# Kernel optimization log

Hardware: AMD Instinct MI355X
Metric: run time of the kernel (lower is better)

Reference implementation:

```python
import jax, jax.numpy as jnp
import numpy as np

B, T, D = 4, 1024, 2048      # batch, tokens, d_model (= Linear out_features)
N, S, H = 8, 8, 8            # n_concepts, gate_rank, degen_rank
ETA = 1.0


def setup_inputs() -> dict:
    key = jax.random.key(0)
    ks = jax.random.split(key, 9)
    return {
        "x": jax.random.normal(ks[0], (B, T, D), jnp.float32),
        # selector params (kaiming-ish then / d_model^2 -> small); use /D for nontrivial values
        "select_weight": jax.random.normal(ks[1], (N, D, S), jnp.float32) / D,
        "select_mean_diff": jax.random.normal(ks[2], (N, D), jnp.float32) / D,
        "imp_center": jax.random.normal(ks[3], (N,), jnp.float32),
        "imp_slope": jax.random.normal(ks[4], (N,), jnp.float32) * 5.0,
        "lora_update": jax.random.normal(ks[5], (N, D, H), jnp.float32) * 0.02,
        "lora_degen": jax.random.normal(ks[6], (N, D, H), jnp.float32) * 0.02,
        "bias_w": jax.random.normal(ks[7], (N, D), jnp.float32) * 0.02,
        "debias_w": jax.random.normal(ks[8], (N, D), jnp.float32) * 0.02,
    }


def reference(x, select_weight, select_mean_diff, imp_center, imp_slope,
              lora_update, lora_degen, bias_w, debias_w):
    # ---- SimpleSelectorOutProp ----
    # x: [B,T,D]; x_diff: [B,N,T,D]  (x.unsqueeze(1) - mean_diff[None,:,None,:])
    x_diff = x[:, None, :, :] - select_mean_diff[None, :, None, :]
    x_diff = x_diff / jnp.linalg.norm(x_diff, axis=3, keepdims=True)
    # cont: [B,N,T,S] = einsum('nds,bntd->bnts')**2
    cont = jnp.einsum('nds,bntd->bnts', select_weight, x_diff) ** 2
    score = cont.sum(axis=-1)                                   # [B,N,T]
    gate = jax.nn.sigmoid(imp_slope[None, :, None] * (score - imp_center[None, :, None]))
    sel_scale = gate.max(axis=1)[..., None]                     # [B,T,1] (max over concepts)
    sel_idx = gate.argmax(axis=1)                               # [B,T] int (top-1 concept)

    # ---- top-1 concept gather + low-rank update ----
    debias = jnp.take(debias_w, sel_idx, axis=0)                # [B,T,D]
    bias = jnp.take(bias_w, sel_idx, axis=0)                    # [B,T,D]
    upd = jnp.take(lora_update, sel_idx, axis=0)                # [B,T,D,H]
    dgn = jnp.take(lora_degen, sel_idx, axis=0)                 # [B,T,D,H]

    x_debias = x - debias
    mod_x = jnp.einsum('btdh,btd->bth', upd, x_debias)          # [B,T,H]
    degen_up = jnp.einsum('btdh,bth->btd', dgn, mod_x)          # [B,T,D]
    mod_x_bias = ETA * (bias + degen_up)

    # gated residual blend: (1 - s) * x + s * mod_x_bias
    return (1.0 - sel_scale) * x + sel_scale * mod_x_bias
```

## Files before the change

### kernel.cpp

```cpp
#include <hip/hip_runtime.h>
#include <math.h>

typedef unsigned short u16;
typedef unsigned int   u32;
typedef unsigned long long u64;
typedef __attribute__((ext_vector_type(4))) unsigned short u16x4;
typedef __attribute__((ext_vector_type(8))) unsigned short bf16x8;
typedef __attribute__((ext_vector_type(8))) short sh8;
typedef __attribute__((ext_vector_type(4))) float f32x4;

#define BT     4096
#define D      2048
#define NC     8
#define NCOL   144
#define NW     16
#define KR     (D / NW)
#define TPB    16
#define LPAD   (NCOL + 4)

__device__ __forceinline__ float bf2f(u16 v) {
    u32 u = ((u32)v) << 16;
    float f; __builtin_memcpy(&f, &u, 4); return f;
}
__device__ __forceinline__ u16 f2bf(float f) {
    u32 u; __builtin_memcpy(&u, &f, 4);
    u += 0x7fffu + ((u >> 16) & 1);
    return (u16)(u >> 16);
}

__device__ __forceinline__ int detect_fp32(const void* xv) {
    const u16* p = (const u16*)xv;
    int l = threadIdx.x & 63;
    bool bad = false;
#pragma unroll
    for (int i = 0; i < 4; i++) {
        float v = bf2f(p[l * 4 + i]);
        if (!(fabsf(v) < 1e4f)) bad = true;
    }
    return __ballot(bad) != 0ull;
}

template<int DT> struct IO;
template<> struct IO<0> {
    static __device__ __forceinline__ float ld1(const void* p, size_t i) {
        return bf2f(((const u16*)p)[i]);
    }
    static __device__ __forceinline__ void ld4(const void* p, size_t i, float* o) {
        u16x4 v = *(const u16x4*)((const u16*)p + i);
#pragma unroll
        for (int k = 0; k < 4; k++) o[k] = bf2f(v[k]);
    }
    static __device__ __forceinline__ void ld8(const void* p, size_t i, float* o) {
        bf16x8 v = *(const bf16x8*)((const u16*)p + i);
#pragma unroll
        for (int k = 0; k < 8; k++) o[k] = bf2f(v[k]);
    }
    static __device__ __forceinline__ void st4(void* p, size_t i, const float* v) {
        u16x4 o;
#pragma unroll
        for (int k = 0; k < 4; k++) o[k] = f2bf(v[k]);
        *(u16x4*)((u16*)p + i) = o;
    }
    static __device__ __forceinline__ u16 ldbf(const void* p, size_t i) {
        return ((const u16*)p)[i];
    }
    static __device__ __forceinline__ sh8 afrag(const void* p, size_t i) {
        return *(const sh8*)((const u16*)p + i);
    }
};
template<> struct IO<1> {
    static __device__ __forceinline__ float ld1(const void* p, size_t i) {
        return ((const float*)p)[i];
    }
    static __device__ __forceinline__ void ld4(const void* p, size_t i, float* o) {
        f32x4 a = *(const f32x4*)((const float*)p + i);
#pragma unroll
        for (int k = 0; k < 4; k++) o[k] = a[k];
    }
    static __device__ __forceinline__ void ld8(const void* p, size_t i, float* o) {
        f32x4 a = *(const f32x4*)((const float*)p + i);
        f32x4 b = *(const f32x4*)((const float*)p + i + 4);
#pragma unroll
        for (int k = 0; k < 4; k++) { o[k] = a[k]; o[4 + k] = b[k]; }
    }
    static __device__ __forceinline__ void st4(void* p, size_t i, const float* v) {
        f32x4 a;
#pragma unroll
        for (int k = 0; k < 4; k++) a[k] = v[k];
        *(f32x4*)((float*)p + i) = a;
    }
    static __device__ __forceinline__ u16 ldbf(const void* p, size_t i) {
        return f2bf(((const float*)p)[i]);
    }
    static __device__ __forceinline__ sh8 afrag(const void* p, size_t i) {
        f32x4 a = *(const f32x4*)((const float*)p + i);
        f32x4 b = *(const f32x4*)((const float*)p + i + 4);
        sh8 r;
#pragma unroll
        for (int k = 0; k < 4; k++) {
            r[k]     = (short)f2bf(a[k]);
            r[4 + k] = (short)f2bf(b[k]);
        }
        return r;
    }
};

template<int DT>
__device__ __forceinline__ void prep_part(const void* selW, const void* upd,
                                          const void* mu, u16* __restrict__ WtT) {
    int idx = blockIdx.x * 256 + threadIdx.x;
    int j = idx >> 8, d0 = (idx & 255) * 8;
    bf16x8 v;
    if (j < 64) {
        int n = j >> 3, s = j & 7;
#pragma unroll
        for (int i = 0; i < 8; i++) v[i] = IO<DT>::ldbf(selW, ((size_t)n * D + d0 + i) * 8 + s);
    } else if (j < 128) {
        int n = (j - 64) >> 3, h = j & 7;
#pragma unroll
        for (int i = 0; i < 8; i++) v[i] = IO<DT>::ldbf(upd, ((size_t)n * D + d0 + i) * 8 + h);
    } else if (j < 136) {
#pragma unroll
        for (int i = 0; i < 8; i++) v[i] = IO<DT>::ldbf(mu, (size_t)(j - 128) * D + d0 + i);
    } else {
#pragma unroll
        for (int i = 0; i < 8; i++) v[i] = 0;
    }
    *(bf16x8*)(WtT + (size_t)j * D + d0) = v;
}

template<int DT>
__device__ __forceinline__ void consts_part(const void* W, const void* mu,
                                            const void* upd, const void* deb,
                                            float* __restrict__ gPart) {
    int pid = blockIdx.x - 144;
    int n = pid >> 3, t = threadIdx.x;
    int d = (pid & 7) * 256 + t;

    float mud = IO<DT>::ld1(mu,  (size_t)n * D + d);
    float dbd = IO<DT>::ld1(deb, (size_t)n * D + d);
    float m2 = mud * mud;
    float wv[8], uv[8], o[8], u[8];
    IO<DT>::ld8(W,   ((size_t)n * D + d) * 8, wv);
    IO<DT>::ld8(upd, ((size_t)n * D + d) * 8, uv);
#pragma unroll
    for (int s = 0; s < 8; s++) { o[s] = wv[s] * mud; u[s] = uv[s] * dbd; }

#pragma unroll
    for (int i = 1; i < 64; i <<= 1) {
        m2 += __shfl_xor(m2, i, 64);
#pragma unroll
        for (int s = 0; s < 8; s++) {
            o[s] += __shfl_xor(o[s], i, 64);
            u[s] += __shfl_xor(u[s], i, 64);
        }
    }
    __shared__ float red[4][17];
    int wave = t >> 6, lane = t & 63;
    if (lane == 0) {
        red[wave][0] = m2;
#pragma unroll
        for (int s = 0; s < 8; s++) { red[wave][1 + s] = o[s]; red[wave][9 + s] = u[s]; }
    }
    __syncthreads();
    if (t < 17) {
        float acc = red[0][t] + red[1][t] + red[2][t] + red[3][t];
        gPart[pid * 17 + t] = acc;
    }
}

template<int DT>
__device__ __forceinline__ void dgnb_part(const void* dgn, u16* __restrict__ dgnb) {
    int idx = (blockIdx.x - 208) * 256 + threadIdx.x;
    float v[8];
    IO<DT>::ld8(dgn, (size_t)idx * 8, v);
    bf16x8 o;
#pragma unroll
    for (int k = 0; k < 8; k++) o[k] = f2bf(v[k]);
    *(bf16x8*)(dgnb + (size_t)idx * 8) = o;
}

__global__ __launch_bounds__(256) void k_prep(
    const void* x, const void* selW, const void* upd, const void* mu,
    const void* deb, const void* dgn, u16* WtT, float* gPart, u16* dgnb) {
    int f = detect_fp32(x);
    if (blockIdx.x < 144) {
        if (f) prep_part<1>(selW, upd, mu, WtT); else prep_part<0>(selW, upd, mu, WtT);
    } else if (blockIdx.x < 208) {
        if (f) consts_part<1>(selW, mu, upd, deb, gPart);
        else   consts_part<0>(selW, mu, upd, deb, gPart);
    } else {
        if (f) dgnb_part<1>(dgn, dgnb); else dgnb_part<0>(dgn, dgnb);
    }
}

template<int DT>
__device__ __forceinline__ void fused_body(
    const void* X, const u16* __restrict__ WtT, const float* __restrict__ gPart,
    const u16* __restrict__ DGNB, const void* BIAS,
    const void* CENTER, const void* SLOPE, void* OUT,
    float (*LP)[TPB][LPAD], float (*LS2)[TPB],
    float (*cOFF)[8], float (*cUB)[8], float* cMU2,
    float (*mxL)[8], float* svalL, int* cL) {

    const int t = threadIdx.x;
    const int w = t >> 6, l = t & 63;
    const int m = l & 15, q = l >> 4;
    const int tok0 = blockIdx.x * TPB;
    const int k0 = w * KR;

    if (t < 136) {
        int n = t / 17, k = t % 17;
        float s = 0.f;
#pragma unroll
        for (int j = 0; j < 8; j++) s += gPart[(n * 8 + j) * 17 + k];
        if (k == 0)      cMU2[n] = s;
        else if (k < 9)  cOFF[n][k - 1] = s;
        else             cUB[n][k - 9] = s;
    }

    const size_t aoff = (size_t)(tok0 + m) * D + k0 + q * 8;
    const u16* bp = WtT + (size_t)m * D + k0 + q * 8;

    f32x4 acc[9];
#pragma unroll
    for (int ct = 0; ct < 9; ct++) acc[ct] = (f32x4){0.f, 0.f, 0.f, 0.f};
    float s2 = 0.f;

#pragma unroll 2
    for (int ks = 0; ks < KR / 32; ks++) {
        sh8 a = IO<DT>::afrag(X, aoff + ks * 32);
        sh8 b[9];
#pragma unroll
        for (int ct = 0; ct < 9; ct++)
            b[ct] = *(const sh8*)(bp + (size_t)ct * 16 * D + ks * 32);
#pragma unroll
        for (int i = 0; i < 8; i++) {
            float xv = bf2f((u16)a[i]);
            s2 = fmaf(xv, xv, s2);
        }
#pragma unroll
        for (int ct = 0; ct < 9; ct++)
            acc[ct] = __builtin_amdgcn_mfma_f32_16x16x32_bf16(a, b[ct], acc[ct], 0, 0, 0);
    }

    s2 += __shfl_xor(s2, 16, 64);
    s2 += __shfl_xor(s2, 32, 64);
    if (l < 16) LS2[w][l] = s2;

#pragma unroll
    for (int ct = 0; ct < 9; ct++)
#pragma unroll
        for (int r = 0; r < 4; r++)
            LP[w][q * 4 + r][ct * 16 + m] = acc[ct][r];
    __syncthreads();

    if (t < 128) {
        const int tok = t >> 3, n = t & 7;
        float sx2 = 0.f;
#pragma unroll
        for (int u = 0; u < NW; u++) sx2 += LS2[u][tok];

        float pa[8];
#pragma unroll
        for (int s = 0; s < 8; s++) {
            float v = 0.f;
#pragma unroll
            for (int u = 0; u < NW; u++) v += LP[u][tok][n * 8 + s];
            pa[s] = v;
        }
        float mdot = 0.f;
#pragma unroll
        for (int u = 0; u < NW; u++) mdot += LP[u][tok][128 + n];

        float norm2 = sx2 - 2.f * mdot + cMU2[n];
        float sc = 0.f;
#pragma unroll
        for (int s = 0; s < 8; s++) {
            float dd = pa[s] - cOFF[n][s];
            sc += dd * dd;
        }
        sc /= norm2;
        float zv = IO<DT>::ld1(SLOPE, n) * (sc - IO<DT>::ld1(CENTER, n));
        int iv = n;
#pragma unroll
        for (int i = 1; i < 8; i <<= 1) {
            float z2 = __shfl_xor(zv, i, 64);
            int   i2 = __shfl_xor(iv, i, 64);
            if (z2 > zv || (z2 == zv && i2 < iv)) { zv = z2; iv = i2; }
        }
        const int c = iv;
        float mxv = 0.f;
#pragma unroll
        for (int u = 0; u < NW; u++) mxv += LP[u][tok][64 + c * 8 + n];
        mxL[tok][n] = mxv - cUB[c][n];
        if (n == 0) { svalL[tok] = 1.f / (1.f + expf(-zv)); cL[tok] = c; }
    }
    __syncthreads();

    const int half = t >> 9;
    const int tid  = t & 511;
    const int d0   = tid * 4;
#pragma unroll
    for (int ti = 0; ti < TPB / 2; ++ti) {
        const int tok = half * (TPB / 2) + ti;
        const int c = cL[tok];
        const float sval = svalL[tok];
        float mxa[8];
#pragma unroll
        for (int h = 0; h < 8; h++) mxa[h] = mxL[tok][h];

        const size_t trow = (size_t)(tok0 + tok) * D;
        float xf[4], bv[4], ov[4];
        IO<DT>::ld4(X,    trow + d0, xf);
        IO<DT>::ld4(BIAS, (size_t)c * D + d0, bv);
#pragma unroll
        for (int i = 0; i < 4; i++) {
            bf16x8 v = *(const bf16x8*)(DGNB + ((size_t)c * D + d0 + i) * 8);
            float du = bf2f(v[0]) * mxa[0] + bf2f(v[1]) * mxa[1]
                     + bf2f(v[2]) * mxa[2] + bf2f(v[3]) * mxa[3]
                     + bf2f(v[4]) * mxa[4] + bf2f(v[5]) * mxa[5]
                     + bf2f(v[6]) * mxa[6] + bf2f(v[7]) * mxa[7];
            ov[i] = (1.f - sval) * xf[i] + sval * (bv[i] + du);
        }
        IO<DT>::st4(OUT, trow + d0, ov);
    }
}

__global__ __launch_bounds__(1024) void k_fused(
    const void* X, const u16* WtT, const float* gPart, const u16* DGNB,
    const void* BIAS, const void* CENTER, const void* SLOPE, void* OUT) {
    __shared__ float LP[NW][TPB][LPAD];
    __shared__ float LS2[NW][TPB];
    __shared__ float cOFF[8][8], cUB[8][8], cMU2[8];
    __shared__ float mxL[TPB][8], svalL[TPB];
    __shared__ int   cL[TPB];
    if (detect_fp32(X))
        fused_body<1>(X, WtT, gPart, DGNB, BIAS, CENTER, SLOPE, OUT,
                      LP, LS2, cOFF, cUB, cMU2, mxL, svalL, cL);
    else
        fused_body<0>(X, WtT, gPart, DGNB, BIAS, CENTER, SLOPE, OUT,
                      LP, LS2, cOFF, cUB, cMU2, mxL, svalL, cL);
}

extern "C" void kernel_launch(void* const* d_in, const int* in_sizes, int n_in,
                              void* d_out, int out_size, void* d_ws, size_t ws_size,
                              hipStream_t stream) {
    const void* x      = d_in[0];
    const void* selW   = d_in[1];
    const void* mu     = d_in[2];
    const void* center = d_in[3];
    const void* slope  = d_in[4];
    const void* upd    = d_in[5];
    const void* dgn    = d_in[6];
    const void* biasW  = d_in[7];
    const void* debW   = d_in[8];

    char* ws = (char*)d_ws;
    u16*   WtT   = (u16*)ws;
    u16*   dgnb  = (u16*)(ws + 589824);
    float* gPart = (float*)(ws + 851968);

    k_prep <<<272, 256, 0, stream>>>(x, selW, upd, mu, debW, dgn, WtT, gPart, dgnb);
    k_fused<<<BT / TPB, 1024, 0, stream>>>(x, WtT, gPart, dgnb, biasW, center, slope, d_out);
}
```

Baseline: 130.6 us.

## Merge prep and fused kernels into one cooperative launch with grid sync

Combines the weight-prep kernel and the main fused kernel into a single cooperative kernel that does a grid-wide sync between phases, removing one launch and its inter-kernel gap. The GEMM split moves from 16 K-slices to 8 K-slices times 2 column groups, and the loads for the next step are software-prefetched. Tokens are also reordered by selected concept before the output pass to improve locality of the gathered degen weights. The cooperative launch needs all 256 blocks of 1024 threads to be co-resident, and the grid barrier has its own cost.

```diff
diff --git a/kernel.cpp b/kernel.cpp
--- a/kernel.cpp
+++ b/kernel.cpp
@@ -1,5 +1,8 @@
 #include <hip/hip_runtime.h>
+#include <hip/hip_cooperative_groups.h>
 #include <math.h>
+
+namespace cg = cooperative_groups;
 
 typedef unsigned short u16;
 typedef unsigned int   u32;
@@ -13,8 +16,8 @@
 #define D      2048
 #define NC     8
 #define NCOL   144
-#define NW     16
-#define KR     (D / NW)
+#define NSL    8
+#define KR     (D / NSL)
 #define TPB    16
 #define LPAD   (NCOL + 4)
 
@@ -106,108 +109,96 @@
 };
 
 template<int DT>
-__device__ __forceinline__ void prep_part(const void* selW, const void* upd,
-                                          const void* mu, u16* __restrict__ WtT) {
-    int idx = blockIdx.x * 256 + threadIdx.x;
-    int j = idx >> 8, d0 = (idx & 255) * 8;
-    bf16x8 v;
-    if (j < 64) {
-        int n = j >> 3, s = j & 7;
-#pragma unroll
-        for (int i = 0; i < 8; i++) v[i] = IO<DT>::ldbf(selW, ((size_t)n * D + d0 + i) * 8 + s);
-    } else if (j < 128) {
-        int n = (j - 64) >> 3, h = j & 7;
-#pragma unroll
-        for (int i = 0; i < 8; i++) v[i] = IO<DT>::ldbf(upd, ((size_t)n * D + d0 + i) * 8 + h);
-    } else if (j < 136) {
-#pragma unroll
-        for (int i = 0; i < 8; i++) v[i] = IO<DT>::ldbf(mu, (size_t)(j - 128) * D + d0 + i);
-    } else {
-#pragma unroll
-        for (int i = 0; i < 8; i++) v[i] = 0;
-    }
-    *(bf16x8*)(WtT + (size_t)j * D + d0) = v;
+__device__ __forceinline__ void prep_phase(const void* selW, const void* upd,
+                                           const void* mu, const void* deb,
+                                           const void* dgn,
+                                           u16* __restrict__ WtT,
+                                           float* __restrict__ gPart,
+                                           u16* __restrict__ dgnb,
+                                           float (*red)[17]) {
+    const int b = blockIdx.x, t = threadIdx.x;
+    if (b < 36) {
+        int j = b * 4 + (t >> 8), d0 = (t & 255) * 8;
+        bf16x8 v;
+        if (j < 64) {
+            int n = j >> 3, s = j & 7;
+#pragma unroll
+            for (int i = 0; i < 8; i++) v[i] = IO<DT>::ldbf(selW, ((size_t)n * D + d0 + i) * 8 + s);
+        } else if (j < 128) {
+            int n = (j - 64) >> 3, h = j & 7;
+#pragma unroll
+            for (int i = 0; i < 8; i++) v[i] = IO<DT>::ldbf(upd, ((size_t)n * D + d0 + i) * 8 + h);
+        } else if (j < 136) {
+#pragma unroll
+            for (int i = 0; i < 8; i++) v[i] = IO<DT>::ldbf(mu, (size_t)(j - 128) * D + d0 + i);
+        } else {
+#pragma unroll
+            for (int i = 0; i < 8; i++) v[i] = 0;
+        }
+        *(bf16x8*)(WtT + (size_t)j * D + d0) = v;
+    } else if (b < 52) {
+        int pid = (b - 36) * 4 + (t >> 8);
+        int n = pid >> 3;
+        int d = (pid & 7) * 256 + (t & 255);
+
+        float mud = IO<DT>::ld1(mu,  (size_t)n * D + d);
+        float dbd = IO<DT>::ld1(deb, (size_t)n * D + d);
+        float m2 = mud * mud;
+        float wv[8], uv[8], o[8], u[8];
+        IO<DT>::ld8(selW, ((size_t)n * D + d) * 8, wv);
+        IO<DT>::ld8(upd,  ((size_t)n * D + d) * 8, uv);
+#pragma unroll
+        for (int s = 0; s < 8; s++) { o[s] = wv[s] * mud; u[s] = uv[s] * dbd; }
+
+#pragma unroll
+        for (int i = 1; i < 64; i <<= 1) {
+            m2 += __shfl_xor(m2, i, 64);
+#pragma unroll
+            for (int s = 0; s < 8; s++) {
+                o[s] += __shfl_xor(o[s], i, 64);
+                u[s] += __shfl_xor(u[s], i, 64);
+            }
+        }
+        if ((t & 63) == 0) {
+            int w = t >> 6;
+            red[w][0] = m2;
+#pragma unroll
+            for (int s = 0; s < 8; s++) { red[w][1 + s] = o[s]; red[w][9 + s] = u[s]; }
+        }
+        __syncthreads();
+        if ((t & 255) < 17) {
+            int g = t >> 8, k = t & 255;
+            float acc = red[g * 4 + 0][k] + red[g * 4 + 1][k]
+                      + red[g * 4 + 2][k] + red[g * 4 + 3][k];
+            gPart[pid * 17 + k] = acc;
+        }
+    } else if (b < 68) {
+        int idx = (b - 52) * 1024 + t;
+        float v[8];
+        IO<DT>::ld8(dgn, (size_t)idx * 8, v);
+        bf16x8 o;
+#pragma unroll
+        for (int k = 0; k < 8; k++) o[k] = f2bf(v[k]);
+        *(bf16x8*)(dgnb + (size_t)idx * 8) = o;
+    }
 }
 
 template<int DT>
-__device__ __forceinline__ void consts_part(const void* W, const void* mu,
-                                            const void* upd, const void* deb,
-                                            float* __restrict__ gPart) {
-    int pid = blockIdx.x - 144;
-    int n = pid >> 3, t = threadIdx.x;
-    int d = (pid & 7) * 256 + t;
-
-    float mud = IO<DT>::ld1(mu,  (size_t)n * D + d);
-    float dbd = IO<DT>::ld1(deb, (size_t)n * D + d);
-    float m2 = mud * mud;
-    float wv[8], uv[8], o[8], u[8];
-    IO<DT>::ld8(W,   ((size_t)n * D + d) * 8, wv);
-    IO<DT>::ld8(upd, ((size_t)n * D + d) * 8, uv);
-#pragma unroll
-    for (int s = 0; s < 8; s++) { o[s] = wv[s] * mud; u[s] = uv[s] * dbd; }
-
-#pragma unroll
-    for (int i = 1; i < 64; i <<= 1) {
-        m2 += __shfl_xor(m2, i, 64);
-#pragma unroll
-        for (int s = 0; s < 8; s++) {
-            o[s] += __shfl_xor(o[s], i, 64);
-            u[s] += __shfl_xor(u[s], i, 64);
-        }
-    }
-    __shared__ float red[4][17];
-    int wave = t >> 6, lane = t & 63;
-    if (lane == 0) {
-        red[wave][0] = m2;
-#pragma unroll
-        for (int s = 0; s < 8; s++) { red[wave][1 + s] = o[s]; red[wave][9 + s] = u[s]; }
-    }
-    __syncthreads();
-    if (t < 17) {
-        float acc = red[0][t] + red[1][t] + red[2][t] + red[3][t];
-        gPart[pid * 17 + t] = acc;
-    }
-}
-
-template<int DT>
-__device__ __forceinline__ void dgnb_part(const void* dgn, u16* __restrict__ dgnb) {
-    int idx = (blockIdx.x - 208) * 256 + threadIdx.x;
-    float v[8];
-    IO<DT>::ld8(dgn, (size_t)idx * 8, v);
-    bf16x8 o;
-#pragma unroll
-    for (int k = 0; k < 8; k++) o[k] = f2bf(v[k]);
-    *(bf16x8*)(dgnb + (size_t)idx * 8) = o;
-}
-
-__global__ __launch_bounds__(256) void k_prep(
-    const void* x, const void* selW, const void* upd, const void* mu,
-    const void* deb, const void* dgn, u16* WtT, float* gPart, u16* dgnb) {
-    int f = detect_fp32(x);
-    if (blockIdx.x < 144) {
-        if (f) prep_part<1>(selW, upd, mu, WtT); else prep_part<0>(selW, upd, mu, WtT);
-    } else if (blockIdx.x < 208) {
-        if (f) consts_part<1>(selW, mu, upd, deb, gPart);
-        else   consts_part<0>(selW, mu, upd, deb, gPart);
-    } else {
-        if (f) dgnb_part<1>(dgn, dgnb); else dgnb_part<0>(dgn, dgnb);
-    }
-}
-
-template<int DT>
-__device__ __forceinline__ void fused_body(
+__device__ __forceinline__ void fused_phase(
     const void* X, const u16* __restrict__ WtT, const float* __restrict__ gPart,
     const u16* __restrict__ DGNB, const void* BIAS,
     const void* CENTER, const void* SLOPE, void* OUT,
     float (*LP)[TPB][LPAD], float (*LS2)[TPB],
     float (*cOFF)[8], float (*cUB)[8], float* cMU2,
-    float (*mxL)[8], float* svalL, int* cL) {
+    float (*mxL)[8], float* svalL, int* cL, int* ordL) {
 
     const int t = threadIdx.x;
     const int w = t >> 6, l = t & 63;
     const int m = l & 15, q = l >> 4;
     const int tok0 = blockIdx.x * TPB;
-    const int k0 = w * KR;
+    const int kslice = w & 7, ctg = w >> 3;
+    const int k0 = kslice * KR;
+    const int ctbase = ctg * 4;
 
     if (t < 136) {
         int n = t / 17, k = t % 17;
@@ -220,58 +211,71 @@
     }
 
     const size_t aoff = (size_t)(tok0 + m) * D + k0 + q * 8;
-    const u16* bp = WtT + (size_t)m * D + k0 + q * 8;
-
-    f32x4 acc[9];
-#pragma unroll
-    for (int ct = 0; ct < 9; ct++) acc[ct] = (f32x4){0.f, 0.f, 0.f, 0.f};
+    const u16* bp = WtT + (size_t)(m + ctbase * 16) * D + k0 + q * 8;
+
+    f32x4 acc[5];
+#pragma unroll
+    for (int j = 0; j < 5; j++) acc[j] = (f32x4){0.f, 0.f, 0.f, 0.f};
     float s2 = 0.f;
 
-#pragma unroll 2
+    sh8 aC, aN, bC[5], bN[5];
+    aC = IO<DT>::afrag(X, aoff);
+#pragma unroll
+    for (int j = 0; j < 5; j++) bC[j] = *(const sh8*)(bp + (size_t)j * 16 * D);
+
+#pragma unroll
     for (int ks = 0; ks < KR / 32; ks++) {
-        sh8 a = IO<DT>::afrag(X, aoff + ks * 32);
-        sh8 b[9];
-#pragma unroll
-        for (int ct = 0; ct < 9; ct++)
-            b[ct] = *(const sh8*)(bp + (size_t)ct * 16 * D + ks * 32);
-#pragma unroll
-        for (int i = 0; i < 8; i++) {
-            float xv = bf2f((u16)a[i]);
-            s2 = fmaf(xv, xv, s2);
-        }
-#pragma unroll
-        for (int ct = 0; ct < 9; ct++)
-            acc[ct] = __builtin_amdgcn_mfma_f32_16x16x32_bf16(a, b[ct], acc[ct], 0, 0, 0);
-    }
-
-    s2 += __shfl_xor(s2, 16, 64);
-    s2 += __shfl_xor(s2, 32, 64);
-    if (l < 16) LS2[w][l] = s2;
-
-#pragma unroll
-    for (int ct = 0; ct < 9; ct++)
+        if (ks < KR / 32 - 1) {
+            aN = IO<DT>::afrag(X, aoff + (ks + 1) * 32);
+#pragma unroll
+            for (int j = 0; j < 5; j++)
+                bN[j] = *(const sh8*)(bp + (size_t)j * 16 * D + (ks + 1) * 32);
+        }
+        if (ctg == 0) {
+#pragma unroll
+            for (int i = 0; i < 8; i++) {
+                float xv = bf2f((u16)aC[i]);
+                s2 = fmaf(xv, xv, s2);
+            }
+        }
+#pragma unroll
+        for (int j = 0; j < 5; j++)
+            acc[j] = __builtin_amdgcn_mfma_f32_16x16x32_bf16(aC, bC[j], acc[j], 0, 0, 0);
+        aC = aN;
+#pragma unroll
+        for (int j = 0; j < 5; j++) bC[j] = bN[j];
+    }
+
+    if (ctg == 0) {
+        s2 += __shfl_xor(s2, 16, 64);
+        s2 += __shfl_xor(s2, 32, 64);
+        if (l < 16) LS2[kslice][l] = s2;
+    }
+
+#pragma unroll
+    for (int j = 0; j < 5; j++)
 #pragma unroll
         for (int r = 0; r < 4; r++)
-            LP[w][q * 4 + r][ct * 16 + m] = acc[ct][r];
+            LP[kslice][q * 4 + r][(ctbase + j) * 16 + m] = acc[j][r];
     __syncthreads();
 
     if (t < 128) {
         const int tok = t >> 3, n = t & 7;
         float sx2 = 0.f;
 #pragma unroll
-        for (int u = 0; u < NW; u++) sx2 += LS2[u][tok];
+        for (int u = 0; u < NSL; u++) sx2 += LS2[u][tok];
 
         float pa[8];
 #pragma unroll
         for (int s = 0; s < 8; s++) {
             float v = 0.f;
 #pragma unroll
-            for (int u = 0; u < NW; u++) v += LP[u][tok][n * 8 + s];
+            for (int u = 0; u < NSL; u++) v += LP[u][tok][n * 8 + s];
             pa[s] = v;
         }
         float mdot = 0.f;
 #pragma unroll
-        for (int u = 0; u < NW; u++) mdot += LP[u][tok][128 + n];
+        for (int u = 0; u < NSL; u++) mdot += LP[u][tok][128 + n];
 
         float norm2 = sx2 - 2.f * mdot + cMU2[n];
         float sc = 0.f;
@@ -292,18 +296,29 @@
         const int c = iv;
         float mxv = 0.f;
 #pragma unroll
-        for (int u = 0; u < NW; u++) mxv += LP[u][tok][64 + c * 8 + n];
+        for (int u = 0; u < NSL; u++) mxv += LP[u][tok][64 + c * 8 + n];
         mxL[tok][n] = mxv - cUB[c][n];
         if (n == 0) { svalL[tok] = 1.f / (1.f + expf(-zv)); cL[tok] = c; }
+    }
+    __syncthreads();
+
+    if (t < 16) {
+        int c = cL[t], r = 0;
+#pragma unroll
+        for (int t2 = 0; t2 < 16; ++t2) {
+            int c2 = cL[t2];
+            if (c2 < c || (c2 == c && t2 < t)) r++;
+        }
+        ordL[r] = t;
     }
     __syncthreads();
 
     const int half = t >> 9;
     const int tid  = t & 511;
     const int d0   = tid * 4;
-#pragma unroll
+#pragma unroll 2
     for (int ti = 0; ti < TPB / 2; ++ti) {
-        const int tok = half * (TPB / 2) + ti;
+        const int tok = ordL[half * (TPB / 2) + ti];
         const int c = cL[tok];
         const float sval = svalL[tok];
         float mxa[8];
@@ -327,20 +342,28 @@
     }
 }
 
-__global__ __launch_bounds__(1024) void k_fused(
-    const void* X, const u16* WtT, const float* gPart, const u16* DGNB,
-    const void* BIAS, const void* CENTER, const void* SLOPE, void* OUT) {
-    __shared__ float LP[NW][TPB][LPAD];
-    __shared__ float LS2[NW][TPB];
+__global__ __launch_bounds__(1024, 4) void k_all(
+    const void* x, const void* selW, const void* mu, const void* center,
+    const void* slope, const void* upd, const void* dgn, const void* biasW,
+    const void* debW, u16* WtT, float* gPart, u16* dgnb, void* OUT) {
+    __shared__ float LP[NSL][TPB][LPAD];
+    __shared__ float LS2[NSL][TPB];
     __shared__ float cOFF[8][8], cUB[8][8], cMU2[8];
     __shared__ float mxL[TPB][8], svalL[TPB];
-    __shared__ int   cL[TPB];
-    if (detect_fp32(X))
-        fused_body<1>(X, WtT, gPart, DGNB, BIAS, CENTER, SLOPE, OUT,
-                      LP, LS2, cOFF, cUB, cMU2, mxL, svalL, cL);
-    else
-        fused_body<0>(X, WtT, gPart, DGNB, BIAS, CENTER, SLOPE, OUT,
-                      LP, LS2, cOFF, cUB, cMU2, mxL, svalL, cL);
+    __shared__ int   cL[TPB], ordL[TPB];
+
+    const int f = detect_fp32(x);
+    float (*red)[17] = (float(*)[17])(&LP[0][0][0]);
+
+    if (f) prep_phase<1>(selW, upd, mu, debW, dgn, WtT, gPart, dgnb, red);
+    else   prep_phase<0>(selW, upd, mu, debW, dgn, WtT, gPart, dgnb, red);
+
+    cg::this_grid().sync();
+
+    if (f) fused_phase<1>(x, WtT, gPart, dgnb, biasW, center, slope, OUT,
+                          LP, LS2, cOFF, cUB, cMU2, mxL, svalL, cL, ordL);
+    else   fused_phase<0>(x, WtT, gPart, dgnb, biasW, center, slope, OUT,
+                          LP, LS2, cOFF, cUB, cMU2, mxL, svalL, cL, ordL);
 }
 
 extern "C" void kernel_launch(void* const* d_in, const int* in_sizes, int n_in,
@@ -361,6 +384,11 @@
     u16*   dgnb  = (u16*)(ws + 589824);
     float* gPart = (float*)(ws + 851968);
 
-    k_prep <<<272, 256, 0, stream>>>(x, selW, upd, mu, debW, dgn, WtT, gPart, dgnb);
-    k_fused<<<BT / TPB, 1024, 0, stream>>>(x, WtT, gPart, dgnb, biasW, center, slope, d_out);
-}
+    void* args[13] = {
+        (void*)&x, (void*)&selW, (void*)&mu, (void*)&center, (void*)&slope,
+        (void*)&upd, (void*)&dgn, (void*)&biasW, (void*)&debW,
+        (void*)&WtT, (void*)&gPart, (void*)&dgnb, (void*)&d_out
+    };
+    hipLaunchCooperativeKernel((const void*)k_all, dim3(BT / TPB), dim3(1024),
+                               args, 0, stream);
+}
```

Result: slower. 188.2 us (+44.1%).
